# Kernel optimization log

Measured on AMD Instinct MI355X. Metric: run time of the kernel, lower is better.

## Reference

```python
import jax, jax.numpy as jnp
import numpy as np

B, C, H, W = 4, 256, 64, 64
C8 = C // 8
MH, MW = 256, 256  # mask input resolution


def _conv(x, w, b, pad, dil=1):
    out = jax.lax.conv_general_dilated(
        x, w, window_strides=(1, 1),
        padding=[(pad, pad), (pad, pad)],
        rhs_dilation=(dil, dil),
        dimension_numbers=("NCHW", "OIHW", "NCHW"))
    return out + b[None, :, None, None]


def setup_inputs() -> dict:
    key = jax.random.key(0)
    ks = jax.random.split(key, 16)

    def w_init(k, shape):
        fan_in = shape[1] * shape[2] * shape[3]
        bound = 1.0 / np.sqrt(fan_in)
        return jax.random.uniform(k, shape, jnp.float32, -bound, bound)

    def b_init(k, n, fan_in):
        bound = 1.0 / np.sqrt(fan_in)
        return jax.random.uniform(k, (n,), jnp.float32, -bound, bound)

    return {
        "x": jax.random.normal(ks[0], (B, C, H, W), jnp.float32),
        "mask": jax.random.uniform(ks[1], (B, 1, MH, MW), jnp.float32),
        "w_ctx": w_init(ks[2], (C, C, 7, 7)),   "b_ctx": b_init(ks[3], C, C * 49),
        "w_wide": w_init(ks[4], (C, C, 5, 5)),  "b_wide": b_init(ks[5], C, C * 25),
        "w_comb": w_init(ks[6], (C, 2 * C, 1, 1)), "b_comb": b_init(ks[7], C, 2 * C),
        "w_q": w_init(ks[8], (C8, C, 1, 1)),    "b_q": b_init(ks[9], C8, C),
        "w_k": w_init(ks[10], (C8, C, 1, 1)),   "b_k": b_init(ks[11], C8, C),
        "w_v": w_init(ks[12], (C, C, 1, 1)),    "b_v": b_init(ks[13], C, C),
    }


def reference(x, mask, w_ctx, b_ctx, w_wide, b_wide, w_comb, b_comb,
              w_q, b_q, w_k, b_k, w_v, b_v):
    local_ctx = _conv(x, w_ctx, b_ctx, pad=3, dil=1)          # [B,C,H,W]
    wide_ctx = _conv(x, w_wide, b_wide, pad=6, dil=3)         # [B,C,H,W]
    multi = _conv(jnp.concatenate([local_ctx, wide_ctx], axis=1),
                  w_comb, b_comb, pad=0)                       # [B,C,H,W]

    b, c, h, w = multi.shape
    n = h * w
    q = _conv(multi, w_q, b_q, pad=0).reshape(b, C8, n)        # [B,C/8,N]
    k = _conv(multi, w_k, b_k, pad=0).reshape(b, C8, n)        # [B,C/8,N]
    v = _conv(multi, w_v, b_v, pad=0).reshape(b, c, n)         # [B,C,N]

    scores = jnp.einsum("bcm,bcn->bmn", q, k)                  # [B,N,N]
    attn = jax.nn.softmax(scores, axis=-1)
    out = jnp.einsum("bcn,bmn->bcm", v, attn).reshape(b, c, h, w)

    # nearest-neighbor resize of mask to (h, w), matching torch F.interpolate
    mh, mw = mask.shape[2], mask.shape[3]
    idx_h = (jnp.arange(h) * mh) // h
    idx_w = (jnp.arange(w) * mw) // w
    mask_r = mask[:, :, idx_h][:, :, :, idx_w]                 # [B,1,h,w]

    return out * (1.0 + mask_r)
```

## Files before the change

kernel.cpp:

```cpp
#include <hip/hip_runtime.h>
#include <math.h>

#define BB 4
#define CC 256
#define HH 64
#define WW 64
#define NN 4096

typedef _Float16 f16x8 __attribute__((ext_vector_type(8)));
typedef float f32x4 __attribute__((ext_vector_type(4)));

__global__ __launch_bounds__(256) void pad_kernel(
    const float* __restrict__ x, _Float16* __restrict__ xpad)
{
  int blk = blockIdx.x;
  int pr = blk % 76;
  int b  = blk / 76;
  int ci = threadIdx.x;
  int r = pr - 6;
  _Float16* dst = xpad + (((size_t)b*76 + pr)*76)*256 + ci;
  if (r < 0 || r >= HH) {
    for (int pc = 0; pc < 76; ++pc) dst[(size_t)pc*256] = (_Float16)0.f;
  } else {
    const float* src = x + ((size_t)b*CC + ci)*NN + (size_t)r*WW;
    for (int pc = 0; pc < 76; ++pc) {
      int c = pc - 6;
      float v = (c >= 0 && c < WW) ? src[c] : 0.f;
      dst[(size_t)pc*256] = (_Float16)v;
    }
  }
}

__global__ __launch_bounds__(256) void wcvt_kernel(
    const float* __restrict__ src, _Float16* __restrict__ dst, int T)
{
  int co = blockIdx.x;
  int ci = threadIdx.x;
  const float* s = src + ((size_t)co*256 + ci)*T;
  for (int t = 0; t < T; ++t)
    dst[(size_t)t*65536 + co*256 + ci] = (_Float16)s[t];
}

__global__ __launch_bounds__(256) void fcvt_kernel(
    const float* __restrict__ src, _Float16* __restrict__ dst, int n)
{
  int i = blockIdx.x * 256 + threadIdx.x;
  if (i < n) dst[i] = (_Float16)src[i];
}

template<int KS, int DIL>
__global__ __launch_bounds__(512) void conv_mfma_kernel(
    const _Float16* __restrict__ xpad, const _Float16* __restrict__ wb,
    const float* __restrict__ bias, _Float16* __restrict__ ctx_t, int c_off)
{
  __shared__ __align__(16) char xs[2*76*512];

  int blk = blockIdx.x;
  int ytile = blk & 31;
  int cot = (blk >> 5) & 1;
  int b = blk >> 6;
  int y0 = ytile * 2;
  int tid = threadIdx.x;
  int lane = tid & 63;
  int wv = tid >> 6;
  int wco = wv >> 1;
  int wsp = wv & 1;
  int l15 = lane & 15;
  int lg  = lane >> 4;

  f32x4 acc[2][4];
  #pragma unroll
  for (int m = 0; m < 2; ++m)
    #pragma unroll
    for (int n = 0; n < 4; ++n) acc[m][n] = (f32x4){0.f, 0.f, 0.f, 0.f};

  for (int kh = 0; kh < KS; ++kh) {
    int prow = 6 + y0 + (kh - KS/2) * DIL;
    const uint4* src = (const uint4*)(xpad + (((size_t)b*76 + prow)*76)*256);
    __syncthreads();
    #pragma unroll
    for (int i = 0; i < 10; ++i) {
      int ch = tid + i*512;
      if (ch < 4864) {
        uint4 v = src[ch];
        int r = ch >> 5, cq = ch & 31;
        *(uint4*)(xs + r*512 + ((cq << 4) ^ ((r & 7) << 4))) = v;
      }
    }
    __syncthreads();
    for (int kw = 0; kw < KS; ++kw) {
      int dx = (kw - KS/2) * DIL;
      int tap = kh*KS + kw;
      const _Float16* wt = wb + ((size_t)tap << 16)
                              + ((size_t)(cot*128 + wco*32 + l15) << 8) + (lg << 3);
      #pragma unroll
      for (int ks = 0; ks < 8; ++ks) {
        f16x8 a0 = *(const f16x8*)(wt + ks*32);
        f16x8 a1 = *(const f16x8*)(wt + 16*256 + ks*32);
        #pragma unroll
        for (int nf = 0; nf < 4; ++nf) {
          int r = wsp*76 + 6 + nf*16 + l15 + dx;
          f16x8 bf = *(const f16x8*)(xs + r*512 + ((ks*64 + (lg << 4)) ^ ((r & 7) << 4)));
          acc[0][nf] = __builtin_amdgcn_mfma_f32_16x16x32_f16(a0, bf, acc[0][nf], 0, 0, 0);
          acc[1][nf] = __builtin_amdgcn_mfma_f32_16x16x32_f16(a1, bf, acc[1][nf], 0, 0, 0);
        }
      }
    }
  }

  __syncthreads();
  _Float16* ep = (_Float16*)xs;
  #pragma unroll
  for (int m = 0; m < 2; ++m)
    #pragma unroll
    for (int i = 0; i < 4; ++i) {
      int co_l = wco*32 + m*16 + lg*4 + i;
      float bs = bias[cot*128 + co_l];
      #pragma unroll
      for (int nf = 0; nf < 4; ++nf) {
        int n_l = wsp*64 + nf*16 + l15;
        ep[n_l*136 + co_l] = (_Float16)(acc[m][nf][i] + bs);
      }
    }
  __syncthreads();
  const int cbase = c_off + cot*128;
  #pragma unroll
  for (int it = 0; it < 4; ++it) {
    int idx = tid + it*512;
    int n_l = idx >> 4, q = idx & 15;
    f16x8 val = *(const f16x8*)(ep + n_l*136 + q*8);
    *(f16x8*)(ctx_t + ((size_t)b*4096 + (size_t)y0*64 + n_l)*512 + cbase + q*8) = val;
  }
}

template<int K, int O, int BIASMODE>
__global__ __launch_bounds__(64) void gemm_nmajor_kernel(
    const _Float16* __restrict__ A, const _Float16* __restrict__ Wt,
    const float* __restrict__ bias0, const float* __restrict__ bias1,
    _Float16* __restrict__ outh)
{
  int nt = blockIdx.x;
  int ot = blockIdx.y;
  int lane = threadIdx.x;
  int l15 = lane & 15, lg = lane >> 4;
  int n0 = nt*64, o0 = ot*64;
  f32x4 acc[4][4] = {};
  for (int k0 = 0; k0 < K; k0 += 32) {
    f16x8 a[4], bfr[4];
    #pragma unroll
    for (int f = 0; f < 4; ++f)
      a[f] = *(const f16x8*)(A + (size_t)(n0 + f*16 + l15)*K + k0 + lg*8);
    #pragma unroll
    for (int f = 0; f < 4; ++f)
      bfr[f] = *(const f16x8*)(Wt + (size_t)(o0 + f*16 + l15)*K + k0 + lg*8);
    #pragma unroll
    for (int i = 0; i < 4; ++i)
      #pragma unroll
      for (int j = 0; j < 4; ++j)
        acc[i][j] = __builtin_amdgcn_mfma_f32_16x16x32_f16(a[i], bfr[j], acc[i][j], 0, 0, 0);
  }
  #pragma unroll
  for (int i = 0; i < 4; ++i)
    #pragma unroll
    for (int j = 0; j < 4; ++j)
      #pragma unroll
      for (int r = 0; r < 4; ++r) {
        int n = n0 + i*16 + lg*4 + r;
        int o = o0 + j*16 + l15;
        float bs = (BIASMODE == 0) ? bias0[o] : (o < 32 ? bias0[o] : bias1[o - 32]);
        outh[(size_t)n*O + o] = (_Float16)(acc[i][j][r] + bs);
      }
}

__global__ __launch_bounds__(64) void gemm_v_kernel(
    const _Float16* __restrict__ M, const _Float16* __restrict__ Wv,
    const float* __restrict__ bias, _Float16* __restrict__ v)
{
  int nt = blockIdx.x;
  int ct = blockIdx.y;
  int lane = threadIdx.x;
  int l15 = lane & 15, lg = lane >> 4;
  int n0 = nt*64, c0 = ct*64;
  f32x4 acc[4][4] = {};
  for (int k0 = 0; k0 < 256; k0 += 32) {
    f16x8 a[4], bfr[4];
    #pragma unroll
    for (int f = 0; f < 4; ++f)
      a[f] = *(const f16x8*)(Wv + (size_t)(c0 + f*16 + l15)*256 + k0 + lg*8);
    #pragma unroll
    for (int f = 0; f < 4; ++f)
      bfr[f] = *(const f16x8*)(M + (size_t)(n0 + f*16 + l15)*256 + k0 + lg*8);
    #pragma unroll
    for (int i = 0; i < 4; ++i)
      #pragma unroll
      for (int j = 0; j < 4; ++j)
        acc[i][j] = __builtin_amdgcn_mfma_f32_16x16x32_f16(a[i], bfr[j], acc[i][j], 0, 0, 0);
  }
  #pragma unroll
  for (int i = 0; i < 4; ++i)
    #pragma unroll
    for (int j = 0; j < 4; ++j)
      #pragma unroll
      for (int r = 0; r < 4; ++r) {
        int c = c0 + i*16 + lg*4 + r;
        int n_abs = n0 + j*16 + l15;
        int b = n_abs >> 12, n = n_abs & 4095;
        v[((size_t)(b*256 + c))*4096 + n] = (_Float16)(acc[i][j][r] + bias[c]);
      }
}

__global__ __launch_bounds__(256) void attn_stats_kernel(
    const _Float16* __restrict__ qh,
    float* __restrict__ rowmaxP, float* __restrict__ rowsumP)
{
  int blk = blockIdx.x;
  int b = blk >> 7, mt = (blk >> 1) & 63, nh = blk & 1;
  int tid = threadIdx.x, lane = tid & 63, w = tid >> 6;
  int l15 = lane & 15, lg = lane >> 4;
  size_t bN = (size_t)b * 4096;
  int mrow = mt*64 + w*16;
  f16x8 ah = *(const f16x8*)(qh + (bN + mrow + l15)*64 + lg*8);
  float rm[4] = {-3e38f, -3e38f, -3e38f, -3e38f};
  float sm[4] = {0.f, 0.f, 0.f, 0.f};
  for (int n0 = nh*2048; n0 < nh*2048 + 2048; n0 += 16) {
    f16x8 bh = *(const f16x8*)(qh + (bN + n0 + l15)*64 + 32 + lg*8);
    f32x4 s = {};
    s = __builtin_amdgcn_mfma_f32_16x16x32_f16(ah, bh, s, 0, 0, 0);
    #pragma unroll
    for (int i = 0; i < 4; ++i) {
      float nm = fmaxf(rm[i], s[i]);
      sm[i] = sm[i]*__expf(rm[i] - nm) + __expf(s[i] - nm);
      rm[i] = nm;
    }
  }
  #pragma unroll
  for (int off = 1; off <= 8; off <<= 1) {
    #pragma unroll
    for (int i = 0; i < 4; ++i) {
      float rmo = __shfl_xor(rm[i], off);
      float smo = __shfl_xor(sm[i], off);
      float M = fmaxf(rm[i], rmo);
      sm[i] = sm[i]*__expf(rm[i] - M) + smo*__expf(rmo - M);
      rm[i] = M;
    }
  }
  if (l15 == 0) {
    #pragma unroll
    for (int i = 0; i < 4; ++i) {
      size_t idx = (size_t)nh*16384 + bN + mrow + lg*4 + i;
      rowmaxP[idx] = rm[i];
      rowsumP[idx] = sm[i];
    }
  }
}

__global__ __launch_bounds__(512) void attn_out_kernel(
    const _Float16* __restrict__ qh, const _Float16* __restrict__ v,
    const float* __restrict__ rowmaxP, const float* __restrict__ rowsumP,
    const float* __restrict__ mask, float* __restrict__ out)
{
  __shared__ union U {
    struct { __align__(16) _Float16 vs[256*40]; __align__(16) _Float16 pl[64*40]; } s;
    float epi[256*68];
  } u;
  int blk = blockIdx.x;
  int b = blk >> 6, mt = blk & 63;
  int tid = threadIdx.x, lane = tid & 63, w = tid >> 6;
  int l15 = lane & 15, lg = lane >> 4;
  size_t bN = (size_t)b * 4096;
  int m0 = mt*64;

  int mf = w >> 1, nf2 = w & 1;
  f16x8 ah = *(const f16x8*)(qh + (bN + m0 + mf*16 + l15)*64 + lg*8);
  float rm[4], rsi[4];
  #pragma unroll
  for (int i = 0; i < 4; ++i) {
    size_t m = bN + m0 + mf*16 + lg*4 + i;
    float r0 = rowmaxP[m], r1 = rowmaxP[16384 + m];
    float s0 = rowsumP[m], s1 = rowsumP[16384 + m];
    float M = fmaxf(r0, r1);
    rm[i] = M;
    rsi[i] = 1.0f / (s0*__expf(r0 - M) + s1*__expf(r1 - M));
  }
  int mh = w >> 2, cw = (w & 3)*64;
  f32x4 acc[2][4] = {};
  const _Float16* vb = v + (size_t)b*256*4096;

  for (int n0 = 0; n0 < 4096; n0 += 32) {
    #pragma unroll
    for (int it = 0; it < 2; ++it) {
      int idx = tid + it*512;
      int c = idx >> 2, q = idx & 3;
      *(f16x8*)(u.s.vs + c*40 + q*8) = *(const f16x8*)(vb + (size_t)c*4096 + n0 + q*8);
    }
    {
      f16x8 bh = *(const f16x8*)(qh + (bN + n0 + nf2*16 + l15)*64 + 32 + lg*8);
      f32x4 s = {};
      s = __builtin_amdgcn_mfma_f32_16x16x32_f16(ah, bh, s, 0, 0, 0);
      #pragma unroll
      for (int i = 0; i < 4; ++i) {
        float p = __expf(s[i] - rm[i]) * rsi[i];
        u.s.pl[(mf*16 + lg*4 + i)*40 + nf2*16 + l15] = (_Float16)p;
      }
    }
    __syncthreads();
    {
      f16x8 pa[2], pb[4];
      #pragma unroll
      for (int af = 0; af < 2; ++af)
        pa[af] = *(const f16x8*)(u.s.pl + (mh*32 + af*16 + l15)*40 + lg*8);
      #pragma unroll
      for (int bf = 0; bf < 4; ++bf)
        pb[bf] = *(const f16x8*)(u.s.vs + (cw + bf*16 + l15)*40 + lg*8);
      #pragma unroll
      for (int af = 0; af < 2; ++af)
        #pragma unroll
        for (int bf = 0; bf < 4; ++bf)
          acc[af][bf] = __builtin_amdgcn_mfma_f32_16x16x32_f16(pa[af], pb[bf], acc[af][bf], 0, 0, 0);
    }
    __syncthreads();
  }

  #pragma unroll
  for (int af = 0; af < 2; ++af)
    #pragma unroll
    for (int bf = 0; bf < 4; ++bf)
      #pragma unroll
      for (int r = 0; r < 4; ++r) {
        int c = cw + bf*16 + l15;
        int ml = mh*32 + af*16 + lg*4 + r;
        u.epi[c*68 + ml] = acc[af][bf][r];
      }
  __syncthreads();
  const float* mb = mask + (size_t)b*65536 + (size_t)(mt*4)*256;
  #pragma unroll
  for (int it = 0; it < 8; ++it) {
    int idx = tid + it*512;
    int c = idx >> 4, q = idx & 15;
    f32x4 val = *(const f32x4*)(u.epi + c*68 + q*4);
    f32x4 o4;
    #pragma unroll
    for (int jj = 0; jj < 4; ++jj) {
      int xcol = q*4 + jj;
      o4[jj] = val[jj] * (1.0f + mb[xcol*4]);
    }
    *(f32x4*)(out + ((size_t)b*256 + c)*4096 + m0 + q*4) = o4;
  }
}

extern "C" void kernel_launch(void* const* d_in, const int* in_sizes, int n_in,
                              void* d_out, int out_size, void* d_ws, size_t ws_size,
                              hipStream_t stream)
{
  (void)in_sizes; (void)n_in; (void)out_size; (void)ws_size;
  const float* x      = (const float*)d_in[0];
  const float* mask   = (const float*)d_in[1];
  const float* w_ctx  = (const float*)d_in[2];
  const float* b_ctx  = (const float*)d_in[3];
  const float* w_wide = (const float*)d_in[4];
  const float* b_wide = (const float*)d_in[5];
  const float* w_comb = (const float*)d_in[6];
  const float* b_comb = (const float*)d_in[7];
  const float* w_q    = (const float*)d_in[8];
  const float* b_q    = (const float*)d_in[9];
  const float* w_k    = (const float*)d_in[10];
  const float* b_k    = (const float*)d_in[11];
  const float* w_v    = (const float*)d_in[12];
  const float* b_v    = (const float*)d_in[13];
  float* out = (float*)d_out;

  float* ws = (float*)d_ws;
  _Float16* xpad    = (_Float16*)(ws);
  _Float16* wb7     = (_Float16*)(ws + 2957312);
  _Float16* wb5     = (_Float16*)(ws + 4562944);
  _Float16* ctx_t   = (_Float16*)(ws + 5382144);
  _Float16* wcombH  = (_Float16*)(ws + 9576448);
  _Float16* wqkH    = (_Float16*)(ws + 9641984);
  _Float16* wvH     = (_Float16*)(ws + 9650176);
  _Float16* multi_t = (_Float16*)(ws);
  _Float16* qkt_h   = (_Float16*)(ws + 2097152);
  float*    rowmaxP = ws + 2621440;
  float*    rowsumP = ws + 2654208;
  _Float16* vbuf    = (_Float16*)(ws + 5382144);

  pad_kernel<<<BB*76, 256, 0, stream>>>(x, xpad);
  wcvt_kernel<<<256, 256, 0, stream>>>(w_ctx, wb7, 49);
  wcvt_kernel<<<256, 256, 0, stream>>>(w_wide, wb5, 25);
  fcvt_kernel<<<512, 256, 0, stream>>>(w_comb, wcombH, 131072);
  fcvt_kernel<<<32, 256, 0, stream>>>(w_q, wqkH, 8192);
  fcvt_kernel<<<32, 256, 0, stream>>>(w_k, wqkH + 8192, 8192);
  fcvt_kernel<<<256, 256, 0, stream>>>(w_v, wvH, 65536);

  conv_mfma_kernel<7, 1><<<256, 512, 0, stream>>>(xpad, wb7, b_ctx, ctx_t, 0);
  conv_mfma_kernel<5, 3><<<256, 512, 0, stream>>>(xpad, wb5, b_wide, ctx_t, 256);

  gemm_nmajor_kernel<512, 256, 0><<<dim3(256, 4), 64, 0, stream>>>(
      ctx_t, wcombH, b_comb, nullptr, multi_t);
  gemm_nmajor_kernel<256, 64, 1><<<dim3(256, 1), 64, 0, stream>>>(
      multi_t, wqkH, b_q, b_k, qkt_h);
  gemm_v_kernel<<<dim3(256, 4), 64, 0, stream>>>(multi_t, wvH, b_v, vbuf);

  attn_stats_kernel<<<512, 256, 0, stream>>>(qkt_h, rowmaxP, rowsumP);
  attn_out_kernel<<<256, 512, 0, stream>>>(qkt_h, vbuf, rowmaxP, rowsumP,
                                           mask, out);
}
```

Before: 545.1 us.

## Merge both dilated convs into one launch and prefetch next input row

The 7x7 and dilated 5x5 convolutions now run as a single 512-block kernel that picks the conv variant by block index, so both fill the GPU together instead of as two half-occupancy launches. The shared-memory input-row load is also software-pipelined: the next kernel row's global loads go into registers before the MFMA loop over the current row, hiding global latency. The cost is ten extra uint4 registers per thread, which may raise register pressure and lower occupancy, and a merged kernel whose register use is set by the larger variant.

```diff
diff --git a/kernel.cpp b/kernel.cpp
--- a/kernel.cpp
+++ b/kernel.cpp
@@ -49,13 +49,11 @@
 }
 
 template<int KS, int DIL>
-__global__ __launch_bounds__(512) void conv_mfma_kernel(
-    const _Float16* __restrict__ xpad, const _Float16* __restrict__ wb,
-    const float* __restrict__ bias, _Float16* __restrict__ ctx_t, int c_off)
-{
-  __shared__ __align__(16) char xs[2*76*512];
-
-  int blk = blockIdx.x;
+__device__ __forceinline__ void conv_body(
+    int blk, const _Float16* __restrict__ xpad, const _Float16* __restrict__ wb,
+    const float* __restrict__ bias, _Float16* __restrict__ ctx_t, int c_off,
+    char* xs)
+{
   int ytile = blk & 31;
   int cot = (blk >> 5) & 1;
   int b = blk >> 6;
@@ -74,20 +72,30 @@
     #pragma unroll
     for (int n = 0; n < 4; ++n) acc[m][n] = (f32x4){0.f, 0.f, 0.f, 0.f};
 
-  for (int kh = 0; kh < KS; ++kh) {
+  uint4 pre[10];
+  auto issue = [&](int kh) {
     int prow = 6 + y0 + (kh - KS/2) * DIL;
     const uint4* src = (const uint4*)(xpad + (((size_t)b*76 + prow)*76)*256);
+    #pragma unroll
+    for (int i = 0; i < 10; ++i) {
+      int ch = tid + i*512;
+      if (ch < 4864) pre[i] = src[ch];
+    }
+  };
+
+  issue(0);
+  for (int kh = 0; kh < KS; ++kh) {
     __syncthreads();
     #pragma unroll
     for (int i = 0; i < 10; ++i) {
       int ch = tid + i*512;
       if (ch < 4864) {
-        uint4 v = src[ch];
         int r = ch >> 5, cq = ch & 31;
-        *(uint4*)(xs + r*512 + ((cq << 4) ^ ((r & 7) << 4))) = v;
+        *(uint4*)(xs + r*512 + ((cq << 4) ^ ((r & 7) << 4))) = pre[i];
       }
     }
     __syncthreads();
+    if (kh + 1 < KS) issue(kh + 1);
     for (int kw = 0; kw < KS; ++kw) {
       int dx = (kw - KS/2) * DIL;
       int tap = kh*KS + kw;
@@ -131,6 +139,19 @@
     f16x8 val = *(const f16x8*)(ep + n_l*136 + q*8);
     *(f16x8*)(ctx_t + ((size_t)b*4096 + (size_t)y0*64 + n_l)*512 + cbase + q*8) = val;
   }
+}
+
+__global__ __launch_bounds__(512) void conv_both_kernel(
+    const _Float16* __restrict__ xpad,
+    const _Float16* __restrict__ wb7, const _Float16* __restrict__ wb5,
+    const float* __restrict__ b7, const float* __restrict__ b5,
+    _Float16* __restrict__ ctx_t)
+{
+  __shared__ __align__(16) char xs[2*76*512];
+  if (blockIdx.x < 256)
+    conv_body<7, 1>(blockIdx.x, xpad, wb7, b7, ctx_t, 0, xs);
+  else
+    conv_body<5, 3>(blockIdx.x - 256, xpad, wb5, b5, ctx_t, 256, xs);
 }
 
 template<int K, int O, int BIASMODE>
@@ -391,8 +412,7 @@
   fcvt_kernel<<<32, 256, 0, stream>>>(w_k, wqkH + 8192, 8192);
   fcvt_kernel<<<256, 256, 0, stream>>>(w_v, wvH, 65536);
 
-  conv_mfma_kernel<7, 1><<<256, 512, 0, stream>>>(xpad, wb7, b_ctx, ctx_t, 0);
-  conv_mfma_kernel<5, 3><<<256, 512, 0, stream>>>(xpad, wb5, b_wide, ctx_t, 256);
+  conv_both_kernel<<<512, 512, 0, stream>>>(xpad, wb7, wb5, b_ctx, b_wide, ctx_t);
 
   gemm_nmajor_kernel<512, 256, 0><<<dim3(256, 4), 64, 0, stream>>>(
       ctx_t, wcombH, b_comb, nullptr, multi_t);
```

New measurement: 584.9 us. 1.07x slower.
